# Kernel tuning notes

Measured on AMD Instinct MI355X. Metric: run time of the kernel, lower is better.

The kernel has to match this reference:

```python
import jax, jax.numpy as jnp
import numpy as np

N, L, E, H = 2, 2048, 1024, 16
D = E // H  # head_dimension


def setup_inputs() -> dict:
    key = jax.random.key(0)
    kq, kk, kv, km, kw, kb = jax.random.split(key, 6)
    return {
        "query": jax.random.normal(kq, (N, L, E), dtype=jnp.float32),
        "key": jax.random.normal(kk, (N, L, E), dtype=jnp.float32),
        "value": jax.random.normal(kv, (N, L, E), dtype=jnp.float32),
        "mask": jax.random.randint(km, (N, 1, L, L), 0, 2, dtype=jnp.int32),
        "W_out": jax.random.normal(kw, (E, E), dtype=jnp.float32) / np.float32(np.sqrt(E)),
        "b_out": jax.random.normal(kb, (E,), dtype=jnp.float32) * np.float32(0.02),
    }


def reference(query, key, value, mask, W_out, b_out):
    n, ql, e = query.shape
    # split heads: [N, L, E] -> [N, L, H, D]
    q = query.reshape(n, ql, H, D)
    k = key.reshape(n, key.shape[1], H, D)
    v = value.reshape(n, value.shape[1], H, D)
    # energy: [N, H, Q, K]
    energy = jnp.einsum('nqhd,nkhd->nhqk', q, k)
    energy = jnp.where(mask == 0, jnp.float32(-1e20), energy)
    scale = jnp.float32(E) ** jnp.float32(0.5)
    attention = jax.nn.softmax(energy / scale, axis=3)
    out = jnp.einsum('nhql,nlhd->nqhd', attention, v).reshape(n, ql, H * D)
    # fully_connected_output: torch Linear -> x @ W^T + b
    return out @ W_out.T + b_out
```

## Files before the change

### kernel.cpp

```cpp
#include <hip/hip_runtime.h>
#include <hip/hip_bf16.h>

#define N_ 2
#define L_ 2048
#define E_ 1024
#define H_ 16
#define D_ 64

typedef __attribute__((ext_vector_type(8))) short bf16x8;
typedef __attribute__((ext_vector_type(4))) short bf16x4;
typedef __attribute__((ext_vector_type(4))) float f32x4;

static __device__ __forceinline__ short bfc(float f) {
    union { __bf16 h; short s; } u;
    u.h = (__bf16)f;
    return u.s;
}

static __device__ __forceinline__ void glds16(const void* g, void* l) {
    __builtin_amdgcn_global_load_lds(
        (const __attribute__((address_space(1))) unsigned int*)g,
        (__attribute__((address_space(3))) unsigned int*)l, 16, 0, 0);
}

__global__ __launch_bounds__(256) void pack_kv(
    const float* __restrict__ K, const float* __restrict__ V,
    unsigned short* __restrict__ Kp, unsigned short* __restrict__ Vp)
{
    __shared__ short T[64][72];

    const int bx = blockIdx.x;
    const int kt = bx & 31;
    const int h  = (bx >> 5) & 15;
    const int n  = bx >> 9;
    const int tid = threadIdx.x;
    const int kq = tid >> 4, c4 = tid & 15;

    const size_t inbase = ((size_t)(n * L_) + kt * 64) * E_ + h * D_;
    const size_t obase  = ((size_t)((n * H_ + h) * 32 + kt)) * 4096;

#pragma unroll
    for (int jj = 0; jj < 4; ++jj) {
        const int r = kq + jj * 16;
        const float4 f = *reinterpret_cast<const float4*>(K + inbase + (size_t)r * E_ + c4 * 4);
        bf16x4 w;
        w[0] = bfc(f.x); w[1] = bfc(f.y); w[2] = bfc(f.z); w[3] = bfc(f.w);
        *reinterpret_cast<bf16x4*>(&Kp[obase + r * 64 + ((c4 * 4) ^ ((r & 7) << 3))]) = w;
    }
#pragma unroll
    for (int jj = 0; jj < 4; ++jj) {
        const int k = kq + jj * 16;
        const float4 f = *reinterpret_cast<const float4*>(V + inbase + (size_t)k * E_ + c4 * 4);
        T[c4 * 4 + 0][k] = bfc(f.x);
        T[c4 * 4 + 1][k] = bfc(f.y);
        T[c4 * 4 + 2][k] = bfc(f.z);
        T[c4 * 4 + 3][k] = bfc(f.w);
    }
    __syncthreads();
#pragma unroll
    for (int jj = 0; jj < 2; ++jj) {
        const int d  = (tid >> 3) + jj * 32;
        const int k8 = (tid & 7) * 8;
        const bf16x8 v = *reinterpret_cast<const bf16x8*>(&T[d][k8]);
        *reinterpret_cast<bf16x8*>(&Vp[obase + d * 64 + (k8 ^ ((d & 7) << 3))]) = v;
    }
}

__global__ __launch_bounds__(256) void attn_fwd(
    const unsigned short* __restrict__ Kp, const unsigned short* __restrict__ Vp,
    const float* __restrict__ Q, const int* __restrict__ mask,
    unsigned short* __restrict__ Obf )
{
    __shared__ __align__(16) short K_lds[64 * 64];
    __shared__ __align__(16) short V_lds[64 * 64];
    __shared__ __align__(16) short P_lds[4][16][72];

    const int tid   = threadIdx.x;
    const int lane  = tid & 63;
    const int wave  = tid >> 6;
    const int row16 = lane & 15;
    const int g     = lane >> 4;
    const int sw    = (row16 & 7) << 3;

    const int bx = blockIdx.x;
    const int qt = bx & 31;
    const int h  = (bx >> 5) & 15;
    const int n  = bx >> 9;

    const int q0w = qt * 64 + wave * 16;

    const float SCL = 0.0450842200277801f;

    const float* qptr = Q + ((size_t)(n * L_ + q0w + row16)) * E_ + h * D_;
    bf16x8 qa[2];
#pragma unroll
    for (int c = 0; c < 2; ++c) {
        const float4 f0 = *reinterpret_cast<const float4*>(qptr + 32 * c + 8 * g);
        const float4 f1 = *reinterpret_cast<const float4*>(qptr + 32 * c + 8 * g + 4);
        bf16x8 a;
        a[0] = bfc(f0.x * SCL); a[1] = bfc(f0.y * SCL);
        a[2] = bfc(f0.z * SCL); a[3] = bfc(f0.w * SCL);
        a[4] = bfc(f1.x * SCL); a[5] = bfc(f1.y * SCL);
        a[6] = bfc(f1.z * SCL); a[7] = bfc(f1.w * SCL);
        qa[c] = a;
    }

    f32x4 o[4];
#pragma unroll
    for (int dt = 0; dt < 4; ++dt) { o[dt][0] = 0.f; o[dt][1] = 0.f; o[dt][2] = 0.f; o[dt][3] = 0.f; }
    float lrun = 0.f;

    const int* mrow = mask + (size_t)n * L_ * L_ + (size_t)(q0w + row16) * L_;
    const char* kvb = (const char*)Kp + ((size_t)(n * H_ + h) * 32) * 8192;
    const char* vvb = (const char*)Vp + ((size_t)(n * H_ + h) * 32) * 8192;

    for (int kt = 0; kt < 32; ++kt) {
        int4 mv[4];
#pragma unroll
        for (int t = 0; t < 4; ++t)
            mv[t] = *reinterpret_cast<const int4*>(mrow + kt * 64 + t * 16 + g * 4);

        __syncthreads();
        {
            const char* kg = kvb + (size_t)kt * 8192;
            const char* vg = vvb + (size_t)kt * 8192;
#pragma unroll
            for (int it = 0; it < 2; ++it) {
                const int off = wave * 2048 + it * 1024;
                glds16(kg + off + lane * 16, (char*)K_lds + off);
                glds16(vg + off + lane * 16, (char*)V_lds + off);
            }
        }
        __syncthreads();

        f32x4 s[4];
#pragma unroll
        for (int t = 0; t < 4; ++t) {
            f32x4 acc; acc[0] = 0.f; acc[1] = 0.f; acc[2] = 0.f; acc[3] = 0.f;
#pragma unroll
            for (int c = 0; c < 2; ++c) {
                const bf16x8 kf = *reinterpret_cast<const bf16x8*>(
                    &K_lds[(t * 16 + row16) * 64 + ((32 * c + 8 * g) ^ sw)]);
                acc = __builtin_amdgcn_mfma_f32_16x16x32_bf16(kf, qa[c], acc, 0, 0, 0);
            }
            s[t] = acc;
        }

#pragma unroll
        for (int t = 0; t < 4; ++t) {
            s[t][0] = mv[t].x ? s[t][0] : -3.0e18f;
            s[t][1] = mv[t].y ? s[t][1] : -3.0e18f;
            s[t][2] = mv[t].z ? s[t][2] : -3.0e18f;
            s[t][3] = mv[t].w ? s[t][3] : -3.0e18f;
        }
        float ps = 0.f;
#pragma unroll
        for (int t = 0; t < 4; ++t) {
            const float p0 = exp2f(s[t][0]);
            const float p1 = exp2f(s[t][1]);
            const float p2 = exp2f(s[t][2]);
            const float p3 = exp2f(s[t][3]);
            s[t][0] = p0; s[t][1] = p1; s[t][2] = p2; s[t][3] = p3;
            ps += (p0 + p1) + (p2 + p3);
        }
        lrun += ps;

#pragma unroll
        for (int t = 0; t < 4; ++t) {
            bf16x4 w;
            w[0] = bfc(s[t][0]); w[1] = bfc(s[t][1]);
            w[2] = bfc(s[t][2]); w[3] = bfc(s[t][3]);
            *reinterpret_cast<bf16x4*>(&P_lds[wave][row16][t * 16 + g * 4]) = w;
        }

#pragma unroll
        for (int c = 0; c < 2; ++c) {
            const bf16x8 pb = *reinterpret_cast<const bf16x8*>(
                &P_lds[wave][row16][32 * c + 8 * g]);
#pragma unroll
            for (int dt = 0; dt < 4; ++dt) {
                const bf16x8 va = *reinterpret_cast<const bf16x8*>(
                    &V_lds[(dt * 16 + row16) * 64 + ((32 * c + 8 * g) ^ sw)]);
                o[dt] = __builtin_amdgcn_mfma_f32_16x16x32_bf16(va, pb, o[dt], 0, 0, 0);
            }
        }
    }

    float l = lrun;
    l += __shfl_xor(l, 16);
    l += __shfl_xor(l, 32);
    const float inv = 1.0f / l;
    unsigned short* ob = Obf + (size_t)(n * L_ + q0w + row16) * E_ + h * D_;
#pragma unroll
    for (int dt = 0; dt < 4; ++dt) {
        bf16x4 w;
        w[0] = bfc(o[dt][0] * inv); w[1] = bfc(o[dt][1] * inv);
        w[2] = bfc(o[dt][2] * inv); w[3] = bfc(o[dt][3] * inv);
        *reinterpret_cast<bf16x4*>(&ob[(dt * 16 + g * 4) ^ sw]) = w;
    }
}

__global__ __launch_bounds__(256) void convert_w(
    const float* __restrict__ W, unsigned short* __restrict__ Wb)
{
    const int i = (blockIdx.x * 256 + threadIdx.x) * 4;
    const int row = i >> 10, col = i & 1023;
    const float4 f = *reinterpret_cast<const float4*>(W + i);
    bf16x4 w;
    w[0] = bfc(f.x); w[1] = bfc(f.y); w[2] = bfc(f.z); w[3] = bfc(f.w);
    const int ch = col & ~63, incol = col & 63;
    *reinterpret_cast<bf16x4*>(&Wb[row * 1024 + ch + (incol ^ ((row & 7) << 3))]) = w;
}

__global__ __launch_bounds__(256) void out_proj_bf(
    const unsigned short* __restrict__ A ,
    const unsigned short* __restrict__ Wb ,
    const float* __restrict__ bias, float* __restrict__ Cout)
{
    __shared__ __align__(16) short A_lds[128 * 64];
    __shared__ __align__(16) short W_lds[128 * 64];

    const int tid   = threadIdx.x;
    const int lane  = tid & 63;
    const int wave  = tid >> 6;
    const int row16 = lane & 15;
    const int g     = lane >> 4;
    const int sw    = (row16 & 7) << 3;
    const int wm = wave >> 1, wn = wave & 1;

    const int m0 = (blockIdx.x & 31) * 128;
    const int n0 = (blockIdx.x >> 5) * 128;

    f32x4 acc[4][4];
#pragma unroll
    for (int fm = 0; fm < 4; ++fm)
#pragma unroll
        for (int fn = 0; fn < 4; ++fn) {
            acc[fm][fn][0] = 0.f; acc[fm][fn][1] = 0.f;
            acc[fm][fn][2] = 0.f; acc[fm][fn][3] = 0.f;
        }

    for (int k0 = 0; k0 < 1024; k0 += 64) {
        __syncthreads();
#pragma unroll
        for (int it = 0; it < 4; ++it) {
            const int off = wave * 4096 + it * 1024;
            const int r = (off >> 7) + (lane >> 3);
            const int ib = (lane & 7) * 16;
            glds16((const char*)A + (size_t)(m0 + r) * 2048 + k0 * 2 + ib,
                   (char*)A_lds + off);
            glds16((const char*)Wb + (size_t)(n0 + r) * 2048 + k0 * 2 + ib,
                   (char*)W_lds + off);
        }
        __syncthreads();

#pragma unroll
        for (int c = 0; c < 2; ++c) {
            bf16x8 af[4], wf[4];
#pragma unroll
            for (int f = 0; f < 4; ++f) {
                af[f] = *reinterpret_cast<const bf16x8*>(
                    &A_lds[(wm * 64 + f * 16 + row16) * 64 + ((32 * c + 8 * g) ^ sw)]);
                wf[f] = *reinterpret_cast<const bf16x8*>(
                    &W_lds[(wn * 64 + f * 16 + row16) * 64 + ((32 * c + 8 * g) ^ sw)]);
            }
#pragma unroll
            for (int fm = 0; fm < 4; ++fm)
#pragma unroll
                for (int fn = 0; fn < 4; ++fn)
                    acc[fm][fn] = __builtin_amdgcn_mfma_f32_16x16x32_bf16(
                        af[fm], wf[fn], acc[fm][fn], 0, 0, 0);
        }
    }

#pragma unroll
    for (int fm = 0; fm < 4; ++fm)
#pragma unroll
        for (int fn = 0; fn < 4; ++fn) {
            const int nn = n0 + wn * 64 + fn * 16 + row16;
            const int mm = m0 + wm * 64 + fm * 16 + g * 4;
            const float b = bias[nn];
#pragma unroll
            for (int i = 0; i < 4; ++i)
                Cout[(size_t)(mm + i) * 1024 + nn] = acc[fm][fn][i] + b;
        }
}

__global__ __launch_bounds__(256) void out_proj_wf32(
    const unsigned short* __restrict__ A,
    const float* __restrict__ W,
    const float* __restrict__ bias, float* __restrict__ Cout)
{
    __shared__ __align__(16) short A_lds[128 * 64];
    __shared__ __align__(16) short W_lds[128 * 64];

    const int tid   = threadIdx.x;
    const int lane  = tid & 63;
    const int wave  = tid >> 6;
    const int row16 = lane & 15;
    const int g     = lane >> 4;
    const int sw    = (row16 & 7) << 3;
    const int wm = wave >> 1, wn = wave & 1;

    const int m0 = (blockIdx.x & 31) * 128;
    const int n0 = (blockIdx.x >> 5) * 128;

    f32x4 acc[4][4];
#pragma unroll
    for (int fm = 0; fm < 4; ++fm)
#pragma unroll
        for (int fn = 0; fn < 4; ++fn) {
            acc[fm][fn][0] = 0.f; acc[fm][fn][1] = 0.f;
            acc[fm][fn][2] = 0.f; acc[fm][fn][3] = 0.f;
        }

    for (int k0 = 0; k0 < 1024; k0 += 64) {
        __syncthreads();
#pragma unroll
        for (int it = 0; it < 4; ++it) {
            const int off = wave * 4096 + it * 1024;
            const int r = (off >> 7) + (lane >> 3);
            const int ib = (lane & 7) * 16;
            glds16((const char*)A + (size_t)(m0 + r) * 2048 + k0 * 2 + ib,
                   (char*)A_lds + off);
        }
#pragma unroll
        for (int it = 0; it < 2; ++it) {
            const int idx = tid + it * 256;
            const int r = idx >> 2, c16 = (idx & 3) * 16;
            const float* wp = W + (size_t)(n0 + r) * 1024 + k0 + c16;
            const float4 f0 = *reinterpret_cast<const float4*>(wp);
            const float4 f1 = *reinterpret_cast<const float4*>(wp + 4);
            const float4 f2 = *reinterpret_cast<const float4*>(wp + 8);
            const float4 f3 = *reinterpret_cast<const float4*>(wp + 12);
            bf16x8 w0, w1;
            w0[0] = bfc(f0.x); w0[1] = bfc(f0.y); w0[2] = bfc(f0.z); w0[3] = bfc(f0.w);
            w0[4] = bfc(f1.x); w0[5] = bfc(f1.y); w0[6] = bfc(f1.z); w0[7] = bfc(f1.w);
            w1[0] = bfc(f2.x); w1[1] = bfc(f2.y); w1[2] = bfc(f2.z); w1[3] = bfc(f2.w);
            w1[4] = bfc(f3.x); w1[5] = bfc(f3.y); w1[6] = bfc(f3.z); w1[7] = bfc(f3.w);
            const int swr = (r & 7) << 3;
            *reinterpret_cast<bf16x8*>(&W_lds[r * 64 + (c16 ^ swr)]) = w0;
            *reinterpret_cast<bf16x8*>(&W_lds[r * 64 + ((c16 + 8) ^ swr)]) = w1;
        }
        __syncthreads();

#pragma unroll
        for (int c = 0; c < 2; ++c) {
            bf16x8 af[4], wf[4];
#pragma unroll
            for (int f = 0; f < 4; ++f) {
                af[f] = *reinterpret_cast<const bf16x8*>(
                    &A_lds[(wm * 64 + f * 16 + row16) * 64 + ((32 * c + 8 * g) ^ sw)]);
                wf[f] = *reinterpret_cast<const bf16x8*>(
                    &W_lds[(wn * 64 + f * 16 + row16) * 64 + ((32 * c + 8 * g) ^ sw)]);
            }
#pragma unroll
            for (int fm = 0; fm < 4; ++fm)
#pragma unroll
                for (int fn = 0; fn < 4; ++fn)
                    acc[fm][fn] = __builtin_amdgcn_mfma_f32_16x16x32_bf16(
                        af[fm], wf[fn], acc[fm][fn], 0, 0, 0);
        }
    }

#pragma unroll
    for (int fm = 0; fm < 4; ++fm)
#pragma unroll
        for (int fn = 0; fn < 4; ++fn) {
            const int nn = n0 + wn * 64 + fn * 16 + row16;
            const int mm = m0 + wm * 64 + fm * 16 + g * 4;
            const float b = bias[nn];
#pragma unroll
            for (int i = 0; i < 4; ++i)
                Cout[(size_t)(mm + i) * 1024 + nn] = acc[fm][fn][i] + b;
        }
}

extern "C" void kernel_launch(void* const* d_in, const int* in_sizes, int n_in,
                              void* d_out, int out_size, void* d_ws, size_t ws_size,
                              hipStream_t stream) {
    const float* Q    = (const float*)d_in[0];
    const float* K    = (const float*)d_in[1];
    const float* V    = (const float*)d_in[2];
    const int*   mask = (const int*)d_in[3];
    const float* W    = (const float*)d_in[4];
    const float* b    = (const float*)d_in[5];
    float* out = (float*)d_out;

    unsigned short* Kp = (unsigned short*)d_out;
    unsigned short* Vp = (unsigned short*)d_out + (size_t)4096 * 1024 / 2 * 2;
    unsigned short* Ob = (unsigned short*)d_ws;
    unsigned short* Wb = (unsigned short*)d_ws + (size_t)4096 * 1024;

    pack_kv<<<dim3(1024), dim3(256), 0, stream>>>(K, V, Kp, Vp);
    attn_fwd<<<dim3(1024), dim3(256), 0, stream>>>(Kp, Vp, Q, mask, Ob);

    if (ws_size >= (size_t)(8 + 2) * 1024 * 1024) {
        convert_w<<<dim3(1024), dim3(256), 0, stream>>>(W, Wb);
        out_proj_bf<<<dim3(256), dim3(256), 0, stream>>>(Ob, Wb, b, out);
    } else {
        out_proj_wf32<<<dim3(256), dim3(256), 0, stream>>>(Ob, W, b, out);
    }
}
```

Before: 233.5 us.

## Bit-pack mask, double-buffer K/V, and process 32 query rows per wave

Adds a pack_mask kernel that turns the int32 mask into 64-bit ballot bitmasks, so the attention kernel reads one bit per key position instead of 4 bytes. The attention kernel now handles 128 queries per block (two 16-row tiles per wave), so each K/V tile loaded into LDS is reused across twice as many queries. It also double-buffers the K/V LDS tiles so the next tile's global-to-LDS load overlaps compute, and remaps block order for locality. In exchange it uses more registers and LDS, runs an extra launch, and needs more workspace, keeping the old path as a fallback.

```diff
diff --git a/kernel.cpp b/kernel.cpp
--- a/kernel.cpp
+++ b/kernel.cpp
@@ -66,14 +66,31 @@
     }
 }
 
-__global__ __launch_bounds__(256) void attn_fwd(
+__global__ __launch_bounds__(256) void pack_mask(
+    const int* __restrict__ mask, unsigned long long* __restrict__ Mb)
+{
+    const int tid  = threadIdx.x;
+    const int lane = tid & 63;
+    const int wave = tid >> 6;
+    const int r = blockIdx.x * 4 + wave;
+    const int* src = mask + (size_t)r * L_;
+    unsigned long long* dst = Mb + (size_t)r * 32;
+#pragma unroll 4
+    for (int kt = 0; kt < 32; ++kt) {
+        const int mv = src[kt * 64 + lane];
+        const unsigned long long b = __ballot(mv != 0);
+        if (lane == 0) dst[kt] = b;
+    }
+}
+
+__global__ __launch_bounds__(256, 4) void attn_fwd(
     const unsigned short* __restrict__ Kp, const unsigned short* __restrict__ Vp,
-    const float* __restrict__ Q, const int* __restrict__ mask,
+    const float* __restrict__ Q, const unsigned long long* __restrict__ Mb,
     unsigned short* __restrict__ Obf )
 {
-    __shared__ __align__(16) short K_lds[64 * 64];
-    __shared__ __align__(16) short V_lds[64 * 64];
-    __shared__ __align__(16) short P_lds[4][16][72];
+    __shared__ __align__(16) short K_lds[2][64 * 64];
+    __shared__ __align__(16) short V_lds[2][64 * 64];
+    __shared__ __align__(16) short P_lds[4][32][72];
 
     const int tid   = threadIdx.x;
     const int lane  = tid & 63;
@@ -82,13 +99,173 @@
     const int g     = lane >> 4;
     const int sw    = (row16 & 7) << 3;
 
+    const int bid = blockIdx.x;
+    const int bx  = (bid & 7) * 64 + (bid >> 3);
+    const int qt = bx & 15;
+    const int h  = (bx >> 4) & 15;
+    const int n  = bx >> 8;
+
+    const int q0w = qt * 128 + wave * 32;
+
+    const float SCL = 0.0450842200277801f;
+
+    bf16x8 qa[2][2];
+#pragma unroll
+    for (int hq = 0; hq < 2; ++hq) {
+        const float* qptr = Q + ((size_t)(n * L_ + q0w + hq * 16 + row16)) * E_ + h * D_;
+#pragma unroll
+        for (int c = 0; c < 2; ++c) {
+            const float4 f0 = *reinterpret_cast<const float4*>(qptr + 32 * c + 8 * g);
+            const float4 f1 = *reinterpret_cast<const float4*>(qptr + 32 * c + 8 * g + 4);
+            bf16x8 a;
+            a[0] = bfc(f0.x * SCL); a[1] = bfc(f0.y * SCL);
+            a[2] = bfc(f0.z * SCL); a[3] = bfc(f0.w * SCL);
+            a[4] = bfc(f1.x * SCL); a[5] = bfc(f1.y * SCL);
+            a[6] = bfc(f1.z * SCL); a[7] = bfc(f1.w * SCL);
+            qa[hq][c] = a;
+        }
+    }
+
+    f32x4 o[2][4];
+#pragma unroll
+    for (int hq = 0; hq < 2; ++hq)
+#pragma unroll
+        for (int dt = 0; dt < 4; ++dt) {
+            o[hq][dt][0] = 0.f; o[hq][dt][1] = 0.f;
+            o[hq][dt][2] = 0.f; o[hq][dt][3] = 0.f;
+        }
+    float lrun[2] = {0.f, 0.f};
+
+    const unsigned long long* mrow0 = Mb + ((size_t)(n * L_) + q0w + row16) * 32;
+    const unsigned long long* mrow1 = mrow0 + 16 * 32;
+    const char* kvb = (const char*)Kp + ((size_t)(n * H_ + h) * 32) * 8192;
+    const char* vvb = (const char*)Vp + ((size_t)(n * H_ + h) * 32) * 8192;
+
+    {
+        const int off = wave * 2048;
+        glds16(kvb + off + lane * 16,        (char*)&K_lds[0][0] + off);
+        glds16(kvb + off + 1024 + lane * 16, (char*)&K_lds[0][0] + off + 1024);
+        glds16(vvb + off + lane * 16,        (char*)&V_lds[0][0] + off);
+        glds16(vvb + off + 1024 + lane * 16, (char*)&V_lds[0][0] + off + 1024);
+    }
+    __syncthreads();
+
+    for (int kt = 0; kt < 32; ++kt) {
+        const int cur = kt & 1;
+        if (kt + 1 < 32) {
+            const char* kg = kvb + (size_t)(kt + 1) * 8192;
+            const char* vg = vvb + (size_t)(kt + 1) * 8192;
+            const int off = wave * 2048;
+            glds16(kg + off + lane * 16,        (char*)&K_lds[cur ^ 1][0] + off);
+            glds16(kg + off + 1024 + lane * 16, (char*)&K_lds[cur ^ 1][0] + off + 1024);
+            glds16(vg + off + lane * 16,        (char*)&V_lds[cur ^ 1][0] + off);
+            glds16(vg + off + 1024 + lane * 16, (char*)&V_lds[cur ^ 1][0] + off + 1024);
+        }
+        const unsigned long long mb0 = mrow0[kt];
+        const unsigned long long mb1 = mrow1[kt];
+
+        f32x4 s[2][4];
+#pragma unroll
+        for (int t = 0; t < 4; ++t) {
+            f32x4 a0, a1;
+            a0[0] = 0.f; a0[1] = 0.f; a0[2] = 0.f; a0[3] = 0.f;
+            a1[0] = 0.f; a1[1] = 0.f; a1[2] = 0.f; a1[3] = 0.f;
+#pragma unroll
+            for (int c = 0; c < 2; ++c) {
+                const bf16x8 kf = *reinterpret_cast<const bf16x8*>(
+                    &K_lds[cur][(t * 16 + row16) * 64 + ((32 * c + 8 * g) ^ sw)]);
+                a0 = __builtin_amdgcn_mfma_f32_16x16x32_bf16(kf, qa[0][c], a0, 0, 0, 0);
+                a1 = __builtin_amdgcn_mfma_f32_16x16x32_bf16(kf, qa[1][c], a1, 0, 0, 0);
+            }
+            s[0][t] = a0; s[1][t] = a1;
+        }
+
+#pragma unroll
+        for (int hq = 0; hq < 2; ++hq) {
+            const unsigned long long mb = hq ? mb1 : mb0;
+            const unsigned lo = (unsigned)(mb >> (g * 4));
+            const unsigned hi = (unsigned)(mb >> (32 + g * 4));
+            float ps = 0.f;
+#pragma unroll
+            for (int t = 0; t < 4; ++t) {
+                const unsigned w32 = (t < 2) ? lo : hi;
+                const int base = (t & 1) * 16;
+#pragma unroll
+                for (int i = 0; i < 4; ++i) {
+                    float p = exp2f(s[hq][t][i]);
+                    p = (w32 & (1u << (base + i))) ? p : 0.0f;
+                    s[hq][t][i] = p;
+                    ps += p;
+                }
+            }
+            lrun[hq] += ps;
+#pragma unroll
+            for (int t = 0; t < 4; ++t) {
+                bf16x4 w;
+                w[0] = bfc(s[hq][t][0]); w[1] = bfc(s[hq][t][1]);
+                w[2] = bfc(s[hq][t][2]); w[3] = bfc(s[hq][t][3]);
+                *reinterpret_cast<bf16x4*>(
+                    &P_lds[wave][hq * 16 + row16][(t * 16 + g * 4) ^ sw]) = w;
+            }
+        }
+
+#pragma unroll
+        for (int c = 0; c < 2; ++c) {
+            const bf16x8 pb0 = *reinterpret_cast<const bf16x8*>(
+                &P_lds[wave][row16][(32 * c + 8 * g) ^ sw]);
+            const bf16x8 pb1 = *reinterpret_cast<const bf16x8*>(
+                &P_lds[wave][16 + row16][(32 * c + 8 * g) ^ sw]);
+#pragma unroll
+            for (int dt = 0; dt < 4; ++dt) {
+                const bf16x8 va = *reinterpret_cast<const bf16x8*>(
+                    &V_lds[cur][(dt * 16 + row16) * 64 + ((32 * c + 8 * g) ^ sw)]);
+                o[0][dt] = __builtin_amdgcn_mfma_f32_16x16x32_bf16(va, pb0, o[0][dt], 0, 0, 0);
+                o[1][dt] = __builtin_amdgcn_mfma_f32_16x16x32_bf16(va, pb1, o[1][dt], 0, 0, 0);
+            }
+        }
+
+        __syncthreads();
+    }
+
+#pragma unroll
+    for (int hq = 0; hq < 2; ++hq) {
+        float l = lrun[hq];
+        l += __shfl_xor(l, 16);
+        l += __shfl_xor(l, 32);
+        const float inv = 1.0f / l;
+        unsigned short* ob = Obf + (size_t)(n * L_ + q0w + hq * 16 + row16) * E_ + h * D_;
+#pragma unroll
+        for (int dt = 0; dt < 4; ++dt) {
+            bf16x4 w;
+            w[0] = bfc(o[hq][dt][0] * inv); w[1] = bfc(o[hq][dt][1] * inv);
+            w[2] = bfc(o[hq][dt][2] * inv); w[3] = bfc(o[hq][dt][3] * inv);
+            *reinterpret_cast<bf16x4*>(&ob[(dt * 16 + g * 4) ^ sw]) = w;
+        }
+    }
+}
+
+__global__ __launch_bounds__(256) void attn_fwd_legacy(
+    const unsigned short* __restrict__ Kp, const unsigned short* __restrict__ Vp,
+    const float* __restrict__ Q, const int* __restrict__ mask,
+    unsigned short* __restrict__ Obf)
+{
+    __shared__ __align__(16) short K_lds[64 * 64];
+    __shared__ __align__(16) short V_lds[64 * 64];
+    __shared__ __align__(16) short P_lds[4][16][72];
+
+    const int tid   = threadIdx.x;
+    const int lane  = tid & 63;
+    const int wave  = tid >> 6;
+    const int row16 = lane & 15;
+    const int g     = lane >> 4;
+    const int sw    = (row16 & 7) << 3;
+
     const int bx = blockIdx.x;
     const int qt = bx & 31;
     const int h  = (bx >> 5) & 15;
     const int n  = bx >> 9;
 
     const int q0w = qt * 64 + wave * 16;
-
     const float SCL = 0.0450842200277801f;
 
     const float* qptr = Q + ((size_t)(n * L_ + q0w + row16)) * E_ + h * D_;
@@ -145,7 +322,6 @@
             }
             s[t] = acc;
         }
-
 #pragma unroll
         for (int t = 0; t < 4; ++t) {
             s[t][0] = mv[t].x ? s[t][0] : -3.0e18f;
@@ -164,7 +340,6 @@
             ps += (p0 + p1) + (p2 + p3);
         }
         lrun += ps;
-
 #pragma unroll
         for (int t = 0; t < 4; ++t) {
             bf16x4 w;
@@ -172,7 +347,6 @@
             w[2] = bfc(s[t][2]); w[3] = bfc(s[t][3]);
             *reinterpret_cast<bf16x4*>(&P_lds[wave][row16][t * 16 + g * 4]) = w;
         }
-
 #pragma unroll
         for (int c = 0; c < 2; ++c) {
             const bf16x8 pb = *reinterpret_cast<const bf16x8*>(
@@ -213,8 +387,8 @@
 }
 
 __global__ __launch_bounds__(256) void out_proj_bf(
-    const unsigned short* __restrict__ A ,
-    const unsigned short* __restrict__ Wb ,
+    const unsigned short* __restrict__ A,
+    const unsigned short* __restrict__ Wb,
     const float* __restrict__ bias, float* __restrict__ Cout)
 {
     __shared__ __align__(16) short A_lds[128 * 64];
@@ -388,17 +562,32 @@
     float* out = (float*)d_out;
 
     unsigned short* Kp = (unsigned short*)d_out;
-    unsigned short* Vp = (unsigned short*)d_out + (size_t)4096 * 1024 / 2 * 2;
+    unsigned short* Vp = (unsigned short*)d_out + (size_t)4096 * 1024;
     unsigned short* Ob = (unsigned short*)d_ws;
-    unsigned short* Wb = (unsigned short*)d_ws + (size_t)4096 * 1024;
+
+    const size_t MB1 = (size_t)1024 * 1024;
 
     pack_kv<<<dim3(1024), dim3(256), 0, stream>>>(K, V, Kp, Vp);
-    attn_fwd<<<dim3(1024), dim3(256), 0, stream>>>(Kp, Vp, Q, mask, Ob);
-
-    if (ws_size >= (size_t)(8 + 2) * 1024 * 1024) {
-        convert_w<<<dim3(1024), dim3(256), 0, stream>>>(W, Wb);
-        out_proj_bf<<<dim3(256), dim3(256), 0, stream>>>(Ob, Wb, b, out);
+
+    if (ws_size >= 9 * MB1) {
+        unsigned long long* Mbits = (unsigned long long*)((char*)d_ws + 8 * MB1);
+        pack_mask<<<dim3(1024), dim3(256), 0, stream>>>(mask, Mbits);
+        attn_fwd<<<dim3(512), dim3(256), 0, stream>>>(Kp, Vp, Q, Mbits, Ob);
+        if (ws_size >= 11 * MB1) {
+            unsigned short* Wb = (unsigned short*)((char*)d_ws + 9 * MB1);
+            convert_w<<<dim3(1024), dim3(256), 0, stream>>>(W, Wb);
+            out_proj_bf<<<dim3(256), dim3(256), 0, stream>>>(Ob, Wb, b, out);
+        } else {
+            out_proj_wf32<<<dim3(256), dim3(256), 0, stream>>>(Ob, W, b, out);
+        }
     } else {
-        out_proj_wf32<<<dim3(256), dim3(256), 0, stream>>>(Ob, W, b, out);
-    }
-}
+        attn_fwd_legacy<<<dim3(1024), dim3(256), 0, stream>>>(Kp, Vp, Q, mask, Ob);
+        if (ws_size >= 10 * MB1) {
+            unsigned short* Wb = (unsigned short*)((char*)d_ws + 8 * MB1);
+            convert_w<<<dim3(1024), dim3(256), 0, stream>>>(W, Wb);
+            out_proj_bf<<<dim3(256), dim3(256), 0, stream>>>(Ob, Wb, b, out);
+        } else {
+            out_proj_wf32<<<dim3(256), dim3(256), 0, stream>>>(Ob, W, b, out);
+        }
+    }
+}
```

New measurement: 250.1 us. 7.1% more time.
